# Performance work log

Measured on AMD Instinct MI355X. Metric: run time of the kernel, lower is better.

The kernel has to match this reference:

```python
import jax, jax.numpy as jnp
import numpy as np

N_NODES = 100000
DIM = 128
N_REL = 8
N_EDGES = 640000
LAMDA = 1  # indexes into [x, z1, z2]


def setup_inputs() -> dict:
    key = jax.random.key(0)
    ks = jax.random.split(key, 6)
    x = jax.random.normal(ks[0], (N_NODES, DIM), dtype=jnp.float32)
    edge_index = jax.random.randint(ks[1], (2, N_EDGES), 0, N_NODES, dtype=jnp.int32)
    edge_type = jax.random.randint(ks[2], (N_EDGES,), 0, N_REL, dtype=jnp.int32)
    edge_weight = jax.random.uniform(ks[3], (N_EDGES,), dtype=jnp.float32)
    # xavier_uniform for [R, in, out] weight stacks (fan_in=DIM, fan_out=DIM)
    limit = float(np.sqrt(6.0 / (DIM + DIM)))
    W1 = jax.random.uniform(ks[4], (N_REL, DIM, DIM), jnp.float32, -limit, limit)
    W2 = jax.random.uniform(ks[5], (N_REL, DIM, DIM), jnp.float32, -limit, limit)
    b1 = jnp.zeros((DIM,), jnp.float32)
    b2 = jnp.zeros((DIM,), jnp.float32)
    return {"x": x, "edge_index": edge_index, "edge_type": edge_type,
            "edge_weight": edge_weight, "W1": W1, "b1": b1, "W2": W2, "b2": b2}


def _ecge_conv(x, W, b, row, col, edge_type, coef, n_nodes):
    # Faithful to: msg_e = norm_e * w_e * (x[row_e] @ W[type_e]); out = scatter_add(msg, col) + b
    # Efficient form: transform every node by every relation once (N,R,D), then gather per edge.
    xW = jnp.einsum('ni,rio->nro', x, W)          # [N, R, D]
    msg = xW[row, edge_type] * coef[:, None]       # [E, D]
    out = jax.ops.segment_sum(msg, col, num_segments=n_nodes)
    return out + b


def reference(x, edge_index, edge_type, edge_weight, W1, b1, W2, b2):
    n_nodes = x.shape[0]
    row, col = edge_index[0], edge_index[1]
    # symmetric degree normalization based on destination (col) degree
    deg = jax.ops.segment_sum(jnp.ones_like(edge_weight), col, num_segments=n_nodes)
    deg_inv_sqrt = jnp.where(deg > 0, deg ** -0.5, 0.0)
    norm = deg_inv_sqrt[row] * deg_inv_sqrt[col]
    coef = norm * edge_weight

    z1 = jax.nn.relu(_ecge_conv(x, W1, b1, row, col, edge_type, coef, n_nodes))
    # F.dropout with training=False (eval mode) is identity
    z2 = _ecge_conv(z1, W2, b2, row, col, edge_type, coef, n_nodes)

    z_star = (x + z1 + z2) / 4.0
    temp = [x, z1, z2]
    z_sharp = temp[LAMDA]
    for i in range(LAMDA + 1, 3):
        z_sharp = z_sharp + temp[i]
    z_sharp = z_sharp / (4.0 - LAMDA)
    return (z_star, z_sharp)
```

## Files before the change

### kernel.cpp

```cpp
#include <hip/hip_runtime.h>
#include <hip/hip_bf16.h>
#include <cstdint>
#include <cstddef>

#define DIM  128
#define NREL 8
#define SCB  4096
#define CPB  16

typedef __attribute__((ext_vector_type(8))) short short8;
typedef __attribute__((ext_vector_type(4))) float f32x4;

static inline int cdiv(int a, int b){ return (a + b - 1) / b; }

__device__ inline unsigned short f2bf(float f){
    union { float f; uint32_t u; } v; v.f = f;
    uint32_t u = v.u;
    uint32_t r = (u + 0x7FFFu + ((u >> 16) & 1u)) >> 16;
    return (unsigned short)r;
}
__device__ inline uint32_t pack2(float lo, float hi){
    return (uint32_t)f2bf(lo) | ((uint32_t)f2bf(hi) << 16);
}
__device__ inline float bf2f(uint32_t lo16){
    union { uint32_t u; float f; } v; v.u = lo16 << 16; return v.f;
}
__device__ inline float asf(int u){
    union { int i; float f; } v; v.i = u; return v.f;
}

__global__ __launch_bounds__(256) void k_prep(const float4* __restrict__ x, unsigned short* __restrict__ xb, int n4,
                                              const int* __restrict__ col, const int* __restrict__ et, int E,
                                              int* __restrict__ cnt8, int nb4, int eb,
                                              const float* __restrict__ W1, const float* __restrict__ W2,
                                              unsigned short* __restrict__ wpk){
    int blk = blockIdx.x;
    if (blk < nb4){
        int i = blk * 256 + threadIdx.x;
        if (i >= n4) return;
        float4 v = x[i];
        ushort4 o; o.x = f2bf(v.x); o.y = f2bf(v.y); o.z = f2bf(v.z); o.w = f2bf(v.w);
        *(ushort4*)(xb + (size_t)i * 4) = o;
    } else if (blk < nb4 + eb){
        int e = (blk - nb4) * 256 + threadIdx.x;
        if (e < E) atomicAdd(&cnt8[col[e] * NREL + et[e]], 1);
    } else {
        int b = (blk - nb4 - eb) * 4 + (threadIdx.x >> 6);
        int lane = threadIdx.x & 63;
        int ks = b & 3, nt = (b >> 2) & 7, slot = b >> 5;
        const float* Wsrc = (slot < 8) ? (W1 + (size_t)slot * DIM * DIM)
                                       : (W2 + (size_t)(slot - 8) * DIM * DIM);
        int k0 = ks * 32 + (lane >> 4) * 8;
        int n  = nt * 16 + (lane & 15);
        unsigned short o[8];
        #pragma unroll
        for (int j = 0; j < 8; ++j) o[j] = f2bf(Wsrc[(size_t)(k0 + j) * DIM + n]);
        unsigned short* dst = wpk + ((size_t)b * 64 + lane) * 8;
        #pragma unroll
        for (int j = 0; j < 8; ++j) dst[j] = o[j];
    }
}

__global__ __launch_bounds__(256) void k_colsum(const int* __restrict__ cnt8, int N, int* __restrict__ colCnt){
    int c = blockIdx.x * 256 + threadIdx.x;
    if (c >= N) return;
    int s = 0;
    #pragma unroll
    for (int t = 0; t < NREL; ++t) s += cnt8[c * NREL + t];
    colCnt[c] = s;
}

__global__ __launch_bounds__(256) void k_scan1(const int* __restrict__ cnt, int M, int* __restrict__ bsum){
    int t = threadIdx.x;
    int base = blockIdx.x * SCB + t * 16;
    int s = 0;
    #pragma unroll
    for (int k = 0; k < 16; ++k){
        int i = base + k;
        if (i < M) s += cnt[i];
    }
    #pragma unroll
    for (int o = 1; o < 64; o <<= 1) s += __shfl_xor(s, o);
    __shared__ int wsum[4];
    if ((t & 63) == 0) wsum[t >> 6] = s;
    __syncthreads();
    if (t == 0) bsum[blockIdx.x] = wsum[0] + wsum[1] + wsum[2] + wsum[3];
}

__global__ void k_scan2(int* __restrict__ bsum, int NBS, int* __restrict__ total){
    if (threadIdx.x == 0){
        int a = 0;
        for (int i = 0; i < NBS; ++i){ int v = bsum[i]; bsum[i] = a; a += v; }
        *total = a;
    }
}

__global__ __launch_bounds__(256) void k_scan3(const int* __restrict__ cnt, int M,
                                               const int* __restrict__ bsum, const int* __restrict__ total,
                                               int* __restrict__ startArr, int* __restrict__ pos){
    int t = threadIdx.x;
    int base = blockIdx.x * SCB + t * 16;
    int vals[16];
    int s = 0;
    #pragma unroll
    for (int k = 0; k < 16; ++k){
        int i = base + k;
        vals[k] = (i < M) ? cnt[i] : 0;
        s += vals[k];
    }
    int lane = t & 63, w = t >> 6;
    int v = s;
    #pragma unroll
    for (int o = 1; o < 64; o <<= 1){
        int u = __shfl_up(v, o);
        if (lane >= o) v += u;
    }
    __shared__ int wsum[4];
    if (lane == 63) wsum[w] = v;
    __syncthreads();
    int excl = v - s + bsum[blockIdx.x];
    for (int i = 0; i < w; ++i) excl += wsum[i];
    #pragma unroll
    for (int k = 0; k < 16; ++k){
        int i = base + k;
        if (i < M){ startArr[i] = excl; pos[i] = excl; excl += vals[k]; }
    }
    if (blockIdx.x == 0 && t == 0) startArr[M] = *total;
}

__global__ __launch_bounds__(256) void k_place(const int* __restrict__ row, const int* __restrict__ col,
                                               const int* __restrict__ et, const float* __restrict__ ew,
                                               const int* __restrict__ colCnt,
                                               int E, int* __restrict__ pos8, int2* __restrict__ pkm){
    int e = blockIdx.x * 256 + threadIdx.x;
    if (e >= E) return;
    int r = row[e], c = col[e], t = et[e];
    int dr = colCnt[r], dc = colCnt[c];
    float a = dr > 0 ? rsqrtf((float)dr) : 0.f;
    float b = dc > 0 ? rsqrtf((float)dc) : 0.f;
    float cf = a * b * ew[e];
    int p = atomicAdd(&pos8[c * NREL + t], 1);
    union { float f; int i; } cv; cv.f = cf;
    pkm[p] = make_int2(((c & (CPB - 1)) << 24) | (r << 3) | t, cv.i);
}

template<int MODE>
__global__ __launch_bounds__(512, 8) void k_fused(const unsigned short* __restrict__ xbin,
                                                  const unsigned short* __restrict__ wpk,
                                                  const int* __restrict__ cs8,
                                                  const int2* __restrict__ pkm,
                                                  const float* __restrict__ bias,
                                                  unsigned short* __restrict__ zb,
                                                  const unsigned short* __restrict__ xb2,
                                                  const unsigned short* __restrict__ z1b2,
                                                  float* __restrict__ outS,
                                                  float* __restrict__ outH,
                                                  int N, int wslot){
    __shared__ unsigned short s[CPB * 1024];
    int tid = threadIdx.x;
    int wid = tid >> 6, lane = tid & 63;
    int c0 = blockIdx.x * CPB;

    #pragma unroll
    for (int k = 0; k < 16; ++k) ((uint32_t*)s)[tid + 512 * k] = 0u;
    __syncthreads();

#define FLUSH() *(uint32_t*)((char*)s + flushByte) = pack2(a0, a1)
#define PROC(rt, cf, u) do{                                                       \
        int fk_ = (rt) & 0xFF000007;                                              \
        if (fk_ != fkPrev){                                                       \
            if (fkPrev >= 0) FLUSH();                                             \
            fkPrev = fk_;                                                         \
            int cl_ = ((unsigned)(rt)) >> 24; int t_ = (rt) & 7;                  \
            flushByte = cl_ * 2048 + (((t_ << 8) | (lane << 2)) ^ ((cl_ & 7) << 4)); \
            a0 = 0.f; a1 = 0.f;                                                   \
        }                                                                         \
        a0 = fmaf(cf, bf2f((u) & 0xFFFFu), a0);                                   \
        a1 = fmaf(cf, bf2f((u) >> 16),     a1); }while(0)
#define XROW(mx) ((const uint32_t*)(xbin + ((size_t)(((mx) >> 3) & 0x1FFFFF) << 7)))[lane]

    {
        int c = c0 + wid * 2;
        if (c < N){
            int cHi = c + 2; if (cHi > N) cHi = N;
            int e  = cs8[c * NREL];
            int eE = cs8[cHi * NREL];
            int fkPrev = -1;
            int flushByte = 0;
            float a0 = 0.f, a1 = 0.f;
            while (e < eE){
                int n = eE - e; if (n > 64) n = 64;
                int li = lane < n ? lane : n - 1;
                int2 mv = pkm[e + li];
                int j = 0;
                for (; j + 8 <= n; j += 8){
                    int rt[8]; float cf[8]; uint32_t u[8];
                    #pragma unroll
                    for (int k = 0; k < 8; ++k){
                        rt[k] = __builtin_amdgcn_readlane(mv.x, j + k);
                        cf[k] = asf(__builtin_amdgcn_readlane(mv.y, j + k));
                    }
                    #pragma unroll
                    for (int k = 0; k < 8; ++k) u[k] = XROW(rt[k]);
                    #pragma unroll
                    for (int k = 0; k < 8; ++k) PROC(rt[k], cf[k], u[k]);
                }
                for (; j < n; ++j){
                    int rt = __builtin_amdgcn_readlane(mv.x, j);
                    float cf = asf(__builtin_amdgcn_readlane(mv.y, j));
                    uint32_t u = XROW(rt);
                    PROC(rt, cf, u);
                }
                e += n;
            }
            if (fkPrev >= 0) FLUSH();
        }
    }
#undef PROC
#undef FLUSH
#undef XROW
    __syncthreads();

    int nt = wid;
    f32x4 acc = (f32x4){0,0,0,0};

    int al = lane & 15, ak2 = (lane >> 4) * 16;
    int swz = (al & 7) << 4;
    const char* rowA = (const char*)s + al * 2048;

    const short8* bbase = (const short8*)wpk + (size_t)wslot * 2048 + lane;

    #pragma unroll 4
    for (int ksg = 0; ksg < 32; ++ksg){
        int off = (ksg * 64 + ak2) ^ swz;
        short8 A = *(const short8*)(rowA + off);
        int t = ksg >> 2, ksl = ksg & 3;
        short8 B = (bbase + (size_t)t * 2048)[(nt * 4 + ksl) * 64];
        acc = __builtin_amdgcn_mfma_f32_16x16x32_bf16(A, B, acc, 0, 0, 0);
    }
    __syncthreads();

    float* ot = (float*)s;
    int crb = (lane >> 4) * 4, dcl = lane & 15;
    {
        int d = nt * 16 + dcl;
        float bv = bias[d];
        #pragma unroll
        for (int r = 0; r < 4; ++r){
            int mrow = crb + r;
            float v = acc[r] + bv;
            if (MODE == 0) v = fmaxf(v, 0.f);
            ot[mrow * DIM + d] = v;
        }
    }
    __syncthreads();

    if (MODE == 0){
        if (tid < 256){
            int rowi = tid >> 4, seg = tid & 15;
            int c = c0 + rowi;
            if (c < N){
                const float* src = ot + rowi * DIM + seg * 8;
                uint4 vv;
                vv.x = pack2(src[0], src[1]);
                vv.y = pack2(src[2], src[3]);
                vv.z = pack2(src[4], src[5]);
                vv.w = pack2(src[6], src[7]);
                *(uint4*)(zb + ((size_t)c << 7) + seg * 8) = vv;
            }
        }
    } else {
        int rowi = tid >> 5, q = tid & 31;
        int c = c0 + rowi;
        if (c < N){
            int d0 = q * 4;
            size_t o = ((size_t)c << 7) + d0;
            ushort4 xv4 = *(const ushort4*)(xb2 + o);
            ushort4 zv4 = *(const ushort4*)(z1b2 + o);
            const float* src = ot + rowi * DIM + d0;
            f32x4 S, H;
            {
                float xv = bf2f(xv4.x), z1 = bf2f(zv4.x), v = src[0];
                S.x = (xv + z1 + v) * 0.25f; H.x = (z1 + v) * (1.0f / 3.0f);
            }
            {
                float xv = bf2f(xv4.y), z1 = bf2f(zv4.y), v = src[1];
                S.y = (xv + z1 + v) * 0.25f; H.y = (z1 + v) * (1.0f / 3.0f);
            }
            {
                float xv = bf2f(xv4.z), z1 = bf2f(zv4.z), v = src[2];
                S.z = (xv + z1 + v) * 0.25f; H.z = (z1 + v) * (1.0f / 3.0f);
            }
            {
                float xv = bf2f(xv4.w), z1 = bf2f(zv4.w), v = src[3];
                S.w = (xv + z1 + v) * 0.25f; H.w = (z1 + v) * (1.0f / 3.0f);
            }
            __builtin_nontemporal_store(S, (f32x4*)(outS + o));
            __builtin_nontemporal_store(H, (f32x4*)(outH + o));
        }
    }
}

extern "C" void kernel_launch(void* const* d_in, const int* in_sizes, int n_in,
                              void* d_out, int out_size, void* d_ws, size_t ws_size,
                              hipStream_t stream) {
    const float* x  = (const float*)d_in[0];
    const int*   ei = (const int*)d_in[1];
    const int*   et = (const int*)d_in[2];
    const float* ew = (const float*)d_in[3];
    const float* W1 = (const float*)d_in[4];
    const float* b1 = (const float*)d_in[5];
    const float* W2 = (const float*)d_in[6];
    const float* b2 = (const float*)d_in[7];

    int E = in_sizes[2];
    int N = in_sizes[0] / DIM;
    const int* row = ei;
    const int* col = ei + E;

    float* out = (float*)d_out;
    int ND  = N * DIM;
    int ND4 = ND / 4;
    float* zS = out;
    float* zH = out + ND;

    int M8   = N * NREL;
    int NBS8 = cdiv(M8, SCB);

    char* wsb = (char*)d_ws;
    size_t off = 0;
    auto take = [&](size_t bytes) -> char* {
        char* p = wsb + off;
        off = (off + bytes + 255) & ~(size_t)255;
        return p;
    };
    int*            cnt8     = (int*)           take((size_t)M8 * 4);
    int*            start8   = (int*)           take(((size_t)M8 + 1) * 4);
    int*            pos8     = (int*)           take((size_t)M8 * 4);
    int*            colCnt   = (int*)           take((size_t)N * 4);
    int*            bsum     = (int*)           take(((size_t)NBS8 + 1) * 4);
    int2*           pkm      = (int2*)          take((size_t)E * 8);
    unsigned short* wpk      = (unsigned short*)take((size_t)16 * 2048 * 8 * 2);
    unsigned short* xb       = (unsigned short*)take((size_t)ND * 2);
    unsigned short* z1b      = (unsigned short*)take((size_t)ND * 2);
    int* total = bsum + NBS8;
    (void)n_in; (void)out_size; (void)ws_size;

    hipMemsetAsync(cnt8, 0, (size_t)M8 * 4, stream);

    int eb  = cdiv(E, 256);
    int nb4 = cdiv(ND4, 256);
    int nb  = cdiv(N, 256);
    k_prep  <<<nb4 + eb + 128, 256, 0, stream>>>((const float4*)x, xb, ND4, col, et, E, cnt8, nb4, eb, W1, W2, wpk);
    k_colsum<<<nb, 256, 0, stream>>>(cnt8, N, colCnt);
    k_scan1 <<<NBS8, 256, 0, stream>>>(cnt8, M8, bsum);
    k_scan2 <<<1, 64, 0, stream>>>(bsum, NBS8, total);
    k_scan3 <<<NBS8, 256, 0, stream>>>(cnt8, M8, bsum, total, start8, pos8);
    k_place <<<eb, 256, 0, stream>>>(row, col, et, ew, colCnt, E, pos8, pkm);

    int fb = cdiv(N, CPB);
    k_fused<0><<<fb, 512, 0, stream>>>(xb, wpk, start8, pkm, b1, z1b, nullptr, nullptr, nullptr, nullptr, N, 0);
    k_fused<1><<<fb, 512, 0, stream>>>(z1b, wpk, start8, pkm, b2, nullptr, xb, z1b, zS, zH, N, 8);
}
```

Measured before the change: 276.7 us.

## Drop colsum and scan2 kernels, double fused block to 32 columns

```diff
diff --git a/kernel.cpp b/kernel.cpp
--- a/kernel.cpp
+++ b/kernel.cpp
@@ -6,7 +6,7 @@
 #define DIM  128
 #define NREL 8
 #define SCB  4096
-#define CPB  16
+#define CPB  32
 
 typedef __attribute__((ext_vector_type(8))) short short8;
 typedef __attribute__((ext_vector_type(4))) float f32x4;
@@ -61,15 +61,6 @@
     }
 }
 
-__global__ __launch_bounds__(256) void k_colsum(const int* __restrict__ cnt8, int N, int* __restrict__ colCnt){
-    int c = blockIdx.x * 256 + threadIdx.x;
-    if (c >= N) return;
-    int s = 0;
-    #pragma unroll
-    for (int t = 0; t < NREL; ++t) s += cnt8[c * NREL + t];
-    colCnt[c] = s;
-}
-
 __global__ __launch_bounds__(256) void k_scan1(const int* __restrict__ cnt, int M, int* __restrict__ bsum){
     int t = threadIdx.x;
     int base = blockIdx.x * SCB + t * 16;
@@ -87,16 +78,8 @@
     if (t == 0) bsum[blockIdx.x] = wsum[0] + wsum[1] + wsum[2] + wsum[3];
 }
 
-__global__ void k_scan2(int* __restrict__ bsum, int NBS, int* __restrict__ total){
-    if (threadIdx.x == 0){
-        int a = 0;
-        for (int i = 0; i < NBS; ++i){ int v = bsum[i]; bsum[i] = a; a += v; }
-        *total = a;
-    }
-}
-
 __global__ __launch_bounds__(256) void k_scan3(const int* __restrict__ cnt, int M,
-                                               const int* __restrict__ bsum, const int* __restrict__ total,
+                                               const int* __restrict__ bsum, int NBS,
                                                int* __restrict__ startArr, int* __restrict__ pos){
     int t = threadIdx.x;
     int base = blockIdx.x * SCB + t * 16;
@@ -109,6 +92,16 @@
         s += vals[k];
     }
     int lane = t & 63, w = t >> 6;
+
+    int bp = 0, tp = 0;
+    for (int i = lane; i < NBS; i += 64){
+        int bv = bsum[i];
+        if (i < (int)blockIdx.x) bp += bv;
+        tp += bv;
+    }
+    #pragma unroll
+    for (int o = 1; o < 64; o <<= 1){ bp += __shfl_xor(bp, o); tp += __shfl_xor(tp, o); }
+
     int v = s;
     #pragma unroll
     for (int o = 1; o < 64; o <<= 1){
@@ -118,51 +111,54 @@
     __shared__ int wsum[4];
     if (lane == 63) wsum[w] = v;
     __syncthreads();
-    int excl = v - s + bsum[blockIdx.x];
+    int excl = v - s + bp;
     for (int i = 0; i < w; ++i) excl += wsum[i];
     #pragma unroll
     for (int k = 0; k < 16; ++k){
         int i = base + k;
         if (i < M){ startArr[i] = excl; pos[i] = excl; excl += vals[k]; }
     }
-    if (blockIdx.x == 0 && t == 0) startArr[M] = *total;
+    if (blockIdx.x == (unsigned)(gridDim.x - 1) && t == 0) startArr[M] = tp;
 }
 
 __global__ __launch_bounds__(256) void k_place(const int* __restrict__ row, const int* __restrict__ col,
                                                const int* __restrict__ et, const float* __restrict__ ew,
-                                               const int* __restrict__ colCnt,
+                                               const int* __restrict__ cs8,
                                                int E, int* __restrict__ pos8, int2* __restrict__ pkm){
     int e = blockIdx.x * 256 + threadIdx.x;
     if (e >= E) return;
     int r = row[e], c = col[e], t = et[e];
-    int dr = colCnt[r], dc = colCnt[c];
+    int r8 = r << 3, c8 = c << 3;
+    int dr = cs8[r8 + 8] - cs8[r8];
+    int dc = cs8[c8 + 8] - cs8[c8];
     float a = dr > 0 ? rsqrtf((float)dr) : 0.f;
     float b = dc > 0 ? rsqrtf((float)dc) : 0.f;
     float cf = a * b * ew[e];
-    int p = atomicAdd(&pos8[c * NREL + t], 1);
+    int p = atomicAdd(&pos8[c8 + t], 1);
     union { float f; int i; } cv; cv.f = cf;
     pkm[p] = make_int2(((c & (CPB - 1)) << 24) | (r << 3) | t, cv.i);
 }
 
 template<int MODE>
-__global__ __launch_bounds__(512, 8) void k_fused(const unsigned short* __restrict__ xbin,
-                                                  const unsigned short* __restrict__ wpk,
-                                                  const int* __restrict__ cs8,
-                                                  const int2* __restrict__ pkm,
-                                                  const float* __restrict__ bias,
-                                                  unsigned short* __restrict__ zb,
-                                                  const unsigned short* __restrict__ xb2,
-                                                  const unsigned short* __restrict__ z1b2,
-                                                  float* __restrict__ outS,
-                                                  float* __restrict__ outH,
-                                                  int N, int wslot){
+__global__ __launch_bounds__(1024, 8) void k_fused(const unsigned short* __restrict__ xbin,
+                                                   const unsigned short* __restrict__ wpk,
+                                                   const int* __restrict__ cs8,
+                                                   const int2* __restrict__ pkm,
+                                                   const float* __restrict__ bias,
+                                                   unsigned short* __restrict__ zb,
+                                                   const unsigned short* __restrict__ xb2,
+                                                   const unsigned short* __restrict__ z1b2,
+                                                   float* __restrict__ outS,
+                                                   float* __restrict__ outH,
+                                                   int N, int wslot){
     __shared__ unsigned short s[CPB * 1024];
     int tid = threadIdx.x;
     int wid = tid >> 6, lane = tid & 63;
     int c0 = blockIdx.x * CPB;
 
-    #pragma unroll
-    for (int k = 0; k < 16; ++k) ((uint32_t*)s)[tid + 512 * k] = 0u;
+    uint4 z4 = {0u, 0u, 0u, 0u};
+    #pragma unroll
+    for (int k = 0; k < 4; ++k) ((uint4*)s)[tid + 1024 * k] = z4;
     __syncthreads();
 
 #define FLUSH() *(uint32_t*)((char*)s + flushByte) = pack2(a0, a1)
@@ -221,12 +217,12 @@
 #undef XROW
     __syncthreads();
 
-    int nt = wid;
+    int m = wid >> 3, nt = wid & 7;
     f32x4 acc = (f32x4){0,0,0,0};
 
     int al = lane & 15, ak2 = (lane >> 4) * 16;
     int swz = (al & 7) << 4;
-    const char* rowA = (const char*)s + al * 2048;
+    const char* rowA = (const char*)s + (m * 16 + al) * 2048;
 
     const short8* bbase = (const short8*)wpk + (size_t)wslot * 2048 + lane;
 
@@ -247,7 +243,7 @@
         float bv = bias[d];
         #pragma unroll
         for (int r = 0; r < 4; ++r){
-            int mrow = crb + r;
+            int mrow = m * 16 + crb + r;
             float v = acc[r] + bv;
             if (MODE == 0) v = fmaxf(v, 0.f);
             ot[mrow * DIM + d] = v;
@@ -256,7 +252,7 @@
     __syncthreads();
 
     if (MODE == 0){
-        if (tid < 256){
+        if (tid < 512){
             int rowi = tid >> 4, seg = tid & 15;
             int c = c0 + rowi;
             if (c < N){
@@ -337,28 +333,23 @@
     int*            cnt8     = (int*)           take((size_t)M8 * 4);
     int*            start8   = (int*)           take(((size_t)M8 + 1) * 4);
     int*            pos8     = (int*)           take((size_t)M8 * 4);
-    int*            colCnt   = (int*)           take((size_t)N * 4);
     int*            bsum     = (int*)           take(((size_t)NBS8 + 1) * 4);
     int2*           pkm      = (int2*)          take((size_t)E * 8);
     unsigned short* wpk      = (unsigned short*)take((size_t)16 * 2048 * 8 * 2);
     unsigned short* xb       = (unsigned short*)take((size_t)ND * 2);
     unsigned short* z1b      = (unsigned short*)take((size_t)ND * 2);
-    int* total = bsum + NBS8;
     (void)n_in; (void)out_size; (void)ws_size;
 
     hipMemsetAsync(cnt8, 0, (size_t)M8 * 4, stream);
 
     int eb  = cdiv(E, 256);
     int nb4 = cdiv(ND4, 256);
-    int nb  = cdiv(N, 256);
     k_prep  <<<nb4 + eb + 128, 256, 0, stream>>>((const float4*)x, xb, ND4, col, et, E, cnt8, nb4, eb, W1, W2, wpk);
-    k_colsum<<<nb, 256, 0, stream>>>(cnt8, N, colCnt);
     k_scan1 <<<NBS8, 256, 0, stream>>>(cnt8, M8, bsum);
-    k_scan2 <<<1, 64, 0, stream>>>(bsum, NBS8, total);
-    k_scan3 <<<NBS8, 256, 0, stream>>>(cnt8, M8, bsum, total, start8, pos8);
-    k_place <<<eb, 256, 0, stream>>>(row, col, et, ew, colCnt, E, pos8, pkm);
+    k_scan3 <<<NBS8, 256, 0, stream>>>(cnt8, M8, bsum, NBS8, start8, pos8);
+    k_place <<<eb, 256, 0, stream>>>(row, col, et, ew, start8, E, pos8, pkm);
 
     int fb = cdiv(N, CPB);
-    k_fused<0><<<fb, 512, 0, stream>>>(xb, wpk, start8, pkm, b1, z1b, nullptr, nullptr, nullptr, nullptr, N, 0);
-    k_fused<1><<<fb, 512, 0, stream>>>(z1b, wpk, start8, pkm, b2, nullptr, xb, z1b, zS, zH, N, 8);
-}
+    k_fused<0><<<fb, 1024, 0, stream>>>(xb, wpk, start8, pkm, b1, z1b, nullptr, nullptr, nullptr, nullptr, N, 0);
+    k_fused<1><<<fb, 1024, 0, stream>>>(z1b, wpk, start8, pkm, b2, nullptr, xb, z1b, zS, zH, N, 8);
+}
```

Result: no change. 278.5 us (+0.7%).
